# Performance work log

Measured on AMD Instinct MI355X. Metric: run time of the kernel, lower is better.

## Reference

```python
import jax, jax.numpy as jnp
import numpy as np

B, NQ, NK = 8, 1024, 1024
DQ = DK = DV = 512
H = 8
DS = DV // H
EPS = 1e-4
MAX_ITER = 3
SQRT_V = DV ** 0.25  # sqrt(sqrt(dim_V))


def setup_inputs() -> dict:
    key = jax.random.key(0)
    ks = jax.random.split(key, 8)
    s = 0.02
    return {
        "Q": jax.random.normal(ks[0], (B, NQ, DQ), jnp.float32),
        "K": jax.random.normal(ks[1], (B, NK, DK), jnp.float32),
        "Wq": jax.random.normal(ks[2], (DV, DQ), jnp.float32) * s,
        "bq": jnp.zeros((DV,), jnp.float32),
        "Wk": jax.random.normal(ks[3], (DV, DK), jnp.float32) * s,
        "bk": jnp.zeros((DV,), jnp.float32),
        "Wv": jax.random.normal(ks[4], (DV, DK), jnp.float32) * s,
        "bv": jnp.zeros((DV,), jnp.float32),
        "Wo": jax.random.normal(ks[5], (DV, DV), jnp.float32) * s,
        "bo": jnp.zeros((DV,), jnp.float32),
    }


def _split_heads(x):
    # torch.cat(x.split(ds, 2), 0): head-major stacking along batch
    b, n, _ = x.shape
    return x.reshape(b, n, H, DS).transpose(2, 0, 1, 3).reshape(H * b, n, DS)


def _merge_heads(x, b):
    # torch.cat(x.split(b, 0), 2): inverse of _split_heads
    _, n, ds = x.shape
    return x.reshape(H, b, n, ds).transpose(1, 2, 0, 3).reshape(b, n, H * ds)


def _sinkhorn_plan(x, y):
    # x: [M, P1, d], y: [M, P2, d]; cost = pairwise Euclidean (p=2) distance.
    x2 = jnp.sum(x * x, axis=-1)[:, :, None]
    y2 = jnp.sum(y * y, axis=-1)[:, None, :]
    C = jnp.sqrt(jnp.maximum(x2 + y2 - 2.0 * jnp.einsum("mid,mjd->mij", x, y), 0.0))
    m, p1, p2 = C.shape
    log_a = -jnp.log(jnp.float32(p1))  # uniform marginals
    log_b = -jnp.log(jnp.float32(p2))
    u = jnp.zeros((m, p1), C.dtype)
    v = jnp.zeros((m, p2), C.dtype)
    for _ in range(MAX_ITER):  # fixed small iteration count (max_iter=3)
        u = EPS * (log_a - jax.scipy.special.logsumexp((v[:, None, :] - C) / EPS, axis=2))
        v = EPS * (log_b - jax.scipy.special.logsumexp((u[:, :, None] - C) / EPS, axis=1))
    # transport plan P: [M, P1, P2]
    return jnp.exp((u[:, :, None] + v[:, None, :] - C) / EPS)


def reference(Q, K, Wq, bq, Wk, bk, Wv, bv, Wo, bo):
    q = Q @ Wq.T + bq            # [B, NQ, DV]
    k = K @ Wk.T + bk            # [B, NK, DV]
    v = K @ Wv.T + bv            # [B, NK, DV]
    b = Q.shape[0]
    q_, k_, v_ = _split_heads(q), _split_heads(k), _split_heads(v)  # [H*B, N, DS]
    A = _sinkhorn_plan(q_ / SQRT_V, k_ / SQRT_V)                    # [H*B, NQ, NK]
    O = _merge_heads(q_ + jnp.einsum("mij,mjd->mid", A, v_), b)     # [B, NQ, DV]
    return O + jax.nn.relu(O @ Wo.T + bo)
```

## Files before the change

kernel.cpp:

```cpp
#include <hip/hip_runtime.h>
#include <hip/hip_bf16.h>
#include <math.h>

#define NB 8
#define NN 1024
#define ND 512
#define NH 8
#define NDS 64
#define NM 64
#define LOG_A (-6.93147180559945f)
#define SQRT_V 4.75682846001088f
#define INV_SQRT_V 0.210224103813429f
#define INV_EPS 10000.0f
#define L2E  1.44269504088896f
#define LN2F 0.693147180559945f
#define IEL2 14426.9504088896f

#define SPLIT_ELEMS ((size_t)NM * NN * NDS)
#define W_ELEMS     ((size_t)ND * ND)
#define UV_FLOATS   ((size_t)NM * NN)

typedef unsigned short u16;
typedef unsigned int   u32;
typedef __attribute__((ext_vector_type(8))) short bf16x8;
typedef __attribute__((ext_vector_type(4))) float f32x4;

#define MFMA16(a,b,c) __builtin_amdgcn_mfma_f32_16x16x32_bf16(a,b,c,0,0,0)

__device__ __forceinline__ u16 f2bf_t(float x) {
  return (u16)(__float_as_uint(x) >> 16);
}
__device__ __forceinline__ float bf2f(u16 h) {
  return __uint_as_float(((u32)h) << 16);
}
__device__ __forceinline__ float fast_sqrt(float x) {
  float r;
  asm("v_sqrt_f32 %0, %1" : "=v"(r) : "v"(x));
  return r;
}
__device__ __forceinline__ float fast_exp2(float x) {
  float r;
  asm("v_exp_f32 %0, %1" : "=v"(r) : "v"(x));
  return r;
}
__device__ __forceinline__ float max3f(float a, float b, float c) {
  float r;
  asm("v_max3_f32 %0, %1, %2, %3" : "=v"(r) : "v"(a), "v"(b), "v"(c));
  return r;
}
__device__ __forceinline__ void soft_barrier() {
  asm volatile("s_waitcnt lgkmcnt(0)" ::: "memory");
  __builtin_amdgcn_sched_barrier(0);
  __builtin_amdgcn_s_barrier();
  __builtin_amdgcn_sched_barrier(0);
  asm volatile("" ::: "memory");
}

__global__ __launch_bounds__(256) void k_split(
    const float* __restrict__ X, u16* __restrict__ hi, u16* __restrict__ lo)
{
  const size_t i = ((size_t)blockIdx.x * 256 + threadIdx.x) * 4;
  float4 v = *(const float4*)&X[i];
  const float* vp = (const float*)&v;
  u16 h[4], l[4];
#pragma unroll
  for (int j = 0; j < 4; ++j) {
    h[j] = f2bf_t(vp[j]);
    l[j] = f2bf_t(vp[j] - bf2f(h[j]));
  }
  uint2 ph, pl;
  ph.x = (u32)h[0] | ((u32)h[1] << 16);
  ph.y = (u32)h[2] | ((u32)h[3] << 16);
  pl.x = (u32)l[0] | ((u32)l[1] << 16);
  pl.y = (u32)l[2] | ((u32)l[3] << 16);
  *(uint2*)&hi[i] = ph;
  *(uint2*)&lo[i] = pl;
}

__global__ __launch_bounds__(256, 2) void k_proj_mfma(
    const u16* __restrict__ Xh, const u16* __restrict__ Xl,
    const u16* __restrict__ Wh, const u16* __restrict__ Wl,
    const float* __restrict__ bias, u16* __restrict__ oh,
    u16* __restrict__ ol, u16* __restrict__ oT,
    float* __restrict__ nrm, float scale, int mode)
{
  __shared__ __align__(16) u16 Xhs[2][64][72];
  __shared__ __align__(16) u16 Xls[2][64][72];
  __shared__ __align__(16) u16 Whs[2][64][72];
  __shared__ __align__(16) u16 Wls[2][64][72];
  const int t = threadIdx.x;
  const int r0 = blockIdx.x * 64;
  const int h  = blockIdx.y;
  const int c0 = h * 64;
  const int w = t >> 6, l = t & 63;
  const int c = l & 15, kg = l >> 4;
  const int srow = t >> 2;
  const int skoff = (t & 3) * 16;

  const u16* gxh = &Xh[(size_t)(r0 + srow) * ND + skoff];
  const u16* gxl = &Xl[(size_t)(r0 + srow) * ND + skoff];
  const u16* gwh = &Wh[(size_t)(c0 + srow) * ND + skoff];
  const u16* gwl = &Wl[(size_t)(c0 + srow) * ND + skoff];

  bf16x8 rxh0 = *(const bf16x8*)gxh, rxh1 = *(const bf16x8*)(gxh + 8);
  bf16x8 rxl0 = *(const bf16x8*)gxl, rxl1 = *(const bf16x8*)(gxl + 8);
  bf16x8 rwh0 = *(const bf16x8*)gwh, rwh1 = *(const bf16x8*)(gwh + 8);
  bf16x8 rwl0 = *(const bf16x8*)gwl, rwl1 = *(const bf16x8*)(gwl + 8);

  f32x4 acc[4];
#pragma unroll
  for (int cf = 0; cf < 4; ++cf) acc[cf] = (f32x4){0.f, 0.f, 0.f, 0.f};

  for (int kt = 0; kt < 8; ++kt) {
    const int buf = kt & 1;
    *(bf16x8*)&Xhs[buf][srow][skoff]     = rxh0;
    *(bf16x8*)&Xhs[buf][srow][skoff + 8] = rxh1;
    *(bf16x8*)&Xls[buf][srow][skoff]     = rxl0;
    *(bf16x8*)&Xls[buf][srow][skoff + 8] = rxl1;
    *(bf16x8*)&Whs[buf][srow][skoff]     = rwh0;
    *(bf16x8*)&Whs[buf][srow][skoff + 8] = rwh1;
    *(bf16x8*)&Wls[buf][srow][skoff]     = rwl0;
    *(bf16x8*)&Wls[buf][srow][skoff + 8] = rwl1;
    {
      const int nk = ((kt + 1) & 7) * 64;
      rxh0 = *(const bf16x8*)(gxh + nk); rxh1 = *(const bf16x8*)(gxh + nk + 8);
      rxl0 = *(const bf16x8*)(gxl + nk); rxl1 = *(const bf16x8*)(gxl + nk + 8);
      rwh0 = *(const bf16x8*)(gwh + nk); rwh1 = *(const bf16x8*)(gwh + nk + 8);
      rwl0 = *(const bf16x8*)(gwl + nk); rwl1 = *(const bf16x8*)(gwl + nk + 8);
    }
    soft_barrier();
#pragma unroll
    for (int ks = 0; ks < 2; ++ks) {
      bf16x8 Ah = *(const bf16x8*)&Xhs[buf][w * 16 + c][ks * 32 + kg * 8];
      bf16x8 Al = *(const bf16x8*)&Xls[buf][w * 16 + c][ks * 32 + kg * 8];
#pragma unroll
      for (int cf = 0; cf < 4; ++cf) {
        bf16x8 Bh = *(const bf16x8*)&Whs[buf][cf * 16 + c][ks * 32 + kg * 8];
        bf16x8 Bl = *(const bf16x8*)&Wls[buf][cf * 16 + c][ks * 32 + kg * 8];
        acc[cf] = MFMA16(Ah, Bh, acc[cf]);
        acc[cf] = MFMA16(Ah, Bl, acc[cf]);
        acc[cf] = MFMA16(Al, Bh, acc[cf]);
      }
    }
  }

  const int bb = r0 >> 10;
  const int n0 = r0 & 1023;
  const size_t mrow = (size_t)(h * NB + bb) * NN;
  if (mode != 1) {
    float ns[4] = {0.f, 0.f, 0.f, 0.f};
#pragma unroll
    for (int cf = 0; cf < 4; ++cf) {
      const int col = c0 + cf * 16 + c;
      const float bv = bias[col];
#pragma unroll
      for (int r = 0; r < 4; ++r) {
        float v = (acc[cf][r] + bv) * scale;
        u16 hv = f2bf_t(v);
        ns[r] = fmaf(v, v, ns[r]);
        int n = n0 + w * 16 + kg * 4 + r;
        size_t idx = (mrow + n) * NDS + cf * 16 + c;
        oh[idx] = hv;
        if (mode == 0) ol[idx] = f2bf_t(v - bf2f(hv));
      }
    }
#pragma unroll
    for (int off = 1; off <= 8; off <<= 1)
#pragma unroll
      for (int r = 0; r < 4; ++r) ns[r] += __shfl_xor(ns[r], off);
    if (c == 0) {
#pragma unroll
      for (int r = 0; r < 4; ++r)
        nrm[mrow + n0 + w * 16 + kg * 4 + r] = ns[r];
    }
  } else {
#pragma unroll
    for (int cf = 0; cf < 4; ++cf) {
      const int d = cf * 16 + c;
      const float bv = bias[c0 + d];
      u16 p0 = f2bf_t((acc[cf][0] + bv) * scale);
      u16 p1 = f2bf_t((acc[cf][1] + bv) * scale);
      u16 p2 = f2bf_t((acc[cf][2] + bv) * scale);
      u16 p3 = f2bf_t((acc[cf][3] + bv) * scale);
      uint2 p;
      p.x = (u32)p0 | ((u32)p1 << 16);
      p.y = (u32)p2 | ((u32)p3 << 16);
      *(uint2*)&oT[((size_t)(h * NB + bb) * NDS + d) * NN + n0 + w * 16 + kg * 4] = p;
    }
  }
}

__global__ __launch_bounds__(512, 4) void k_lse_mfma(
    const u16* __restrict__ Ah_, const u16* __restrict__ Bh_,
    const float* __restrict__ Anrm, const float* __restrict__ Bnrm,
    const float* __restrict__ din, float* __restrict__ dout, int first)
{
  __shared__ __align__(16) float din_s[NN];
  __shared__ __align__(16) float y2_s[NN];
  __shared__ __align__(16) u16 Bhs[4][64][72];
  const int t = threadIdx.x;
  const int Lb = blockIdx.x;
  const int xcd = Lb & 7, slot = Lb >> 3;
  const int m = xcd + 8 * (slot >> 3);
  const int a0 = (slot & 7) * 128;

  if (first) {
    *(float2*)&din_s[t * 2] = make_float2(0.f, 0.f);
  } else {
    float2 dv = *(const float2*)&din[(size_t)m * NN + t * 2];
    dv.x *= L2E; dv.y *= L2E;
    *(float2*)&din_s[t * 2] = dv;
  }
  *(float2*)&y2_s[t * 2] = *(const float2*)&Bnrm[(size_t)m * NN + t * 2];

  const int w = t >> 6, l = t & 63;
  const int c = l & 15, kg = l >> 4;
  const int arow = a0 + w * 16;
  const size_t mbase = (size_t)m * NN * NDS;

  const u16* pah = &Ah_[mbase + (size_t)(arow + c) * NDS + kg * 8];
  bf16x8 A0h = *(const bf16x8*)pah;
  bf16x8 A1h = *(const bf16x8*)(pah + 32);

  float x2r[4];
#pragma unroll
  for (int r = 0; r < 4; ++r) x2r[r] = Anrm[(size_t)m * NN + arow + kg * 4 + r];
  float M[4], S[4];
#pragma unroll
  for (int r = 0; r < 4; ++r) { M[r] = -3.0e38f; S[r] = 0.f; }

  const int srow = t >> 3;
  const int skoff = (t & 7) * 8;
  const u16* gh = &Bh_[mbase + (size_t)srow * NDS + skoff];
  bf16x8 r0 = *(const bf16x8*)gh;
  bf16x8 r1 = *(const bf16x8*)(gh + 4096);
  __syncthreads();

  for (int bt = 0; bt < 16; bt += 2) {
    const int p2 = (bt >> 1) & 1;
    *(bf16x8*)&Bhs[p2 * 2 + 0][srow][skoff] = r0;
    *(bf16x8*)&Bhs[p2 * 2 + 1][srow][skoff] = r1;
    {
      r0 = *(const bf16x8*)(gh + (size_t)((bt + 2) & 15) * 4096);
      r1 = *(const bf16x8*)(gh + (size_t)((bt + 3) & 15) * 4096);
    }
    soft_barrier();
#pragma unroll
    for (int sub = 0; sub < 2; ++sub) {
      const int b0 = (bt + sub) * 64;
      const int pl = p2 * 2 + sub;
      f32x4 acc[4];
#pragma unroll
      for (int cf = 0; cf < 4; ++cf) {
        const int bl = cf * 16 + c;
        bf16x8 B0h = *(const bf16x8*)&Bhs[pl][bl][kg * 8];
        bf16x8 B1h = *(const bf16x8*)&Bhs[pl][bl][kg * 8 + 32];
        f32x4 a = {0.f, 0.f, 0.f, 0.f};
        a = MFMA16(A0h, B0h, a);
        a = MFMA16(A1h, B1h, a);
        acc[cf] = a;
      }
      float X[4][4];
#pragma unroll
      for (int cf = 0; cf < 4; ++cf) {
        const int col = b0 + cf * 16 + c;
        const float vb2 = din_s[col];
        const float y2  = y2_s[col];
#pragma unroll
        for (int r = 0; r < 4; ++r) {
          float d2 = fmaf(-2.f, acc[cf][r], x2r[r] + y2);
          float sq = fast_sqrt(fmaxf(d2, 0.f));
          X[cf][r] = fmaf(-IEL2, sq, vb2);
        }
      }
#pragma unroll
      for (int r = 0; r < 4; ++r) {
        float m1 = max3f(X[0][r], X[1][r], X[2][r]);
        float nm = max3f(m1, X[3][r], M[r]);
        float s4 = fast_exp2(X[0][r] - nm) + fast_exp2(X[1][r] - nm)
                 + fast_exp2(X[2][r] - nm) + fast_exp2(X[3][r] - nm);
        S[r] = fmaf(S[r], fast_exp2(M[r] - nm), s4);
        M[r] = nm;
      }
    }
  }
#pragma unroll
  for (int off = 1; off <= 8; off <<= 1) {
#pragma unroll
    for (int r = 0; r < 4; ++r) {
      float Mo = __shfl_xor(M[r], off);
      float So = __shfl_xor(S[r], off);
      float nm = fmaxf(M[r], Mo);
      S[r] = S[r] * fast_exp2(M[r] - nm) + So * fast_exp2(Mo - nm);
      M[r] = nm;
    }
  }
  if (c == 0) {
#pragma unroll
    for (int r = 0; r < 4; ++r)
      dout[(size_t)m * NN + arow + kg * 4 + r] =
          LOG_A - M[r] * LN2F - __logf(S[r]);
  }
}

__global__ __launch_bounds__(512, 4) void k_pv_mfma(
    const u16* __restrict__ qh, const u16* __restrict__ ql,
    const u16* __restrict__ kh, const u16* __restrict__ vT,
    const float* __restrict__ qn, const float* __restrict__ kn,
    const float* __restrict__ ue, const float* __restrict__ ve,
    u16* __restrict__ Oh_, u16* __restrict__ Ol_)
{
  __shared__ __align__(16) float ve_s[NN];
  __shared__ __align__(16) float y2_s[NN];
  __shared__ __align__(16) u16 Bhs[2][64][72];
  __shared__ __align__(16) u16 Vs[2][64][72];
  __shared__ __align__(16) u16 pT[8][16][40];
  const int t = threadIdx.x;
  const int Lb = blockIdx.x;
  const int xcd = Lb & 7, slot = Lb >> 3;
  const int m = xcd + 8 * (slot >> 3);
  const int a0 = (slot & 7) * 128;
  {
    float2 vv = *(const float2*)&ve[(size_t)m * NN + t * 2];
    vv.x *= L2E; vv.y *= L2E;
    *(float2*)&ve_s[t * 2] = vv;
  }
  *(float2*)&y2_s[t * 2] = *(const float2*)&kn[(size_t)m * NN + t * 2];

  const int w = t >> 6, l = t & 63;
  const int c = l & 15, kg = l >> 4;
  const int arow = a0 + w * 16;
  const size_t mbase = (size_t)m * NN * NDS;

  const u16* pah = &qh[mbase + (size_t)(arow + c) * NDS + kg * 8];
  bf16x8 A0h = *(const bf16x8*)pah;
  bf16x8 A1h = *(const bf16x8*)(pah + 32);

  float x2r[4], uer2[4];
#pragma unroll
  for (int r = 0; r < 4; ++r) {
    x2r[r]  = qn[(size_t)m * NN + arow + kg * 4 + r];
    uer2[r] = ue[(size_t)m * NN + arow + kg * 4 + r] * L2E;
  }
  f32x4 pacc[4];
#pragma unroll
  for (int df = 0; df < 4; ++df) pacc[df] = (f32x4){0.f, 0.f, 0.f, 0.f};

  const int srow = t >> 3;
  const int skoff = (t & 7) * 8;
  const u16* gh = &kh[mbase + (size_t)srow * NDS + skoff];
  const u16* gv = &vT[((size_t)m * NDS + srow) * NN + skoff];
  bf16x8 rh = *(const bf16x8*)gh;
  bf16x8 rv = *(const bf16x8*)gv;
  __syncthreads();

  for (int bt = 0; bt < 16; ++bt) {
    const int b0 = bt * 64;
    const int buf = bt & 1;
    *(bf16x8*)&Bhs[buf][srow][skoff] = rh;
    *(bf16x8*)&Vs[buf][srow][skoff]  = rv;
    {
      const int nbt = (bt + 1) & 15;
      rh = *(const bf16x8*)(gh + (size_t)nbt * 4096);
      rv = *(const bf16x8*)(gv + (size_t)nbt * 64);
    }
    soft_barrier();
#pragma unroll
    for (int ph = 0; ph < 2; ++ph) {
      f32x4 acc[2];
#pragma unroll
      for (int q = 0; q < 2; ++q) {
        const int cf = ph * 2 + q;
        const int bl = cf * 16 + c;
        bf16x8 B0h = *(const bf16x8*)&Bhs[buf][bl][kg * 8];
        bf16x8 B1h = *(const bf16x8*)&Bhs[buf][bl][kg * 8 + 32];
        f32x4 a = {0.f, 0.f, 0.f, 0.f};
        a = MFMA16(A0h, B0h, a);
        a = MFMA16(A1h, B1h, a);
        acc[q] = a;
      }
#pragma unroll
      for (int q = 0; q < 2; ++q) {
        const int cf = ph * 2 + q;
        const int col = b0 + cf * 16 + c;
        const float ve2 = ve_s[col];
        const float y2  = y2_s[col];
#pragma unroll
        for (int r = 0; r < 4; ++r) {
          float d2 = fmaf(-2.f, acc[q][r], x2r[r] + y2);
          float sq = fast_sqrt(fmaxf(d2, 0.f));
          float p  = fast_exp2(fmaf(-IEL2, sq, uer2[r] + ve2));
          pT[w][kg * 4 + r][q * 16 + c] = f2bf_t(p);
        }
      }
      bf16x8 Pa = *(const bf16x8*)&pT[w][c][kg * 8];
#pragma unroll
      for (int df = 0; df < 4; ++df) {
        bf16x8 Vb = *(const bf16x8*)&Vs[buf][df * 16 + c][ph * 32 + kg * 8];
        pacc[df] = MFMA16(Pa, Vb, pacc[df]);
      }
    }
  }
#pragma unroll
  for (int df = 0; df < 4; ++df) {
#pragma unroll
    for (int r = 0; r < 4; ++r) {
      int row = arow + kg * 4 + r;
      int d = df * 16 + c;
      size_t qi = mbase + (size_t)row * NDS + d;
      float qv = bf2f(qh[qi]) + bf2f(ql[qi]);
      float o  = fmaf(SQRT_V, qv, pacc[df][r]);
      u16 hv = f2bf_t(o);
      Oh_[qi] = hv;
      Ol_[qi] = f2bf_t(o - bf2f(hv));
    }
  }
}

__global__ __launch_bounds__(256, 2) void k_out_mfma(
    const u16* __restrict__ Oh_, const u16* __restrict__ Ol_,
    const u16* __restrict__ Wh, const u16* __restrict__ Wl,
    const float* __restrict__ bo, float* __restrict__ out)
{
  __shared__ __align__(16) u16 Ahs[2][64][72];
  __shared__ __align__(16) u16 Als[2][64][72];
  __shared__ __align__(16) u16 Whs[2][64][72];
  __shared__ __align__(16) u16 Wls[2][64][72];
  const int t = threadIdx.x;
  const int r0 = blockIdx.x * 64;
  const int c0 = blockIdx.y * 64;
  const int bb = r0 >> 10;
  const int n0 = r0 & 1023;
  const int w = t >> 6, l = t & 63;
  const int c = l & 15, kg = l >> 4;
  const int srow = t >> 2;
  const int skoff = (t & 3) * 16;

  f32x4 acc[4];
#pragma unroll
  for (int cf = 0; cf < 4; ++cf) acc[cf] = (f32x4){0.f, 0.f, 0.f, 0.f};

  bf16x8 rah0, rah1, ral0, ral1, rwh0, rwh1, rwl0, rwl1;
  {
    const size_t ob = ((size_t)(0 * NB + bb) * NN + n0 + srow) * NDS;
    const u16* gah = &Oh_[ob + skoff];
    const u16* gal = &Ol_[ob + skoff];
    const u16* gwh = &Wh[(size_t)(c0 + srow) * ND + skoff];
    const u16* gwl = &Wl[(size_t)(c0 + srow) * ND + skoff];
    rah0 = *(const bf16x8*)gah; rah1 = *(const bf16x8*)(gah + 8);
    ral0 = *(const bf16x8*)gal; ral1 = *(const bf16x8*)(gal + 8);
    rwh0 = *(const bf16x8*)gwh; rwh1 = *(const bf16x8*)(gwh + 8);
    rwl0 = *(const bf16x8*)gwl; rwl1 = *(const bf16x8*)(gwl + 8);
  }

  for (int kt = 0; kt < 8; ++kt) {
    const int buf = kt & 1;
    *(bf16x8*)&Ahs[buf][srow][skoff]     = rah0;
    *(bf16x8*)&Ahs[buf][srow][skoff + 8] = rah1;
    *(bf16x8*)&Als[buf][srow][skoff]     = ral0;
    *(bf16x8*)&Als[buf][srow][skoff + 8] = ral1;
    *(bf16x8*)&Whs[buf][srow][skoff]     = rwh0;
    *(bf16x8*)&Whs[buf][srow][skoff + 8] = rwh1;
    *(bf16x8*)&Wls[buf][srow][skoff]     = rwl0;
    *(bf16x8*)&Wls[buf][srow][skoff + 8] = rwl1;
    {
      const int nkt = (kt + 1) & 7;
      const size_t ob = ((size_t)(nkt * NB + bb) * NN + n0 + srow) * NDS;
      const u16* gah = &Oh_[ob + skoff];
      const u16* gal = &Ol_[ob + skoff];
      const u16* gwh = &Wh[(size_t)(c0 + srow) * ND + nkt * 64 + skoff];
      const u16* gwl = &Wl[(size_t)(c0 + srow) * ND + nkt * 64 + skoff];
      rah0 = *(const bf16x8*)gah; rah1 = *(const bf16x8*)(gah + 8);
      ral0 = *(const bf16x8*)gal; ral1 = *(const bf16x8*)(gal + 8);
      rwh0 = *(const bf16x8*)gwh; rwh1 = *(const bf16x8*)(gwh + 8);
      rwl0 = *(const bf16x8*)gwl; rwl1 = *(const bf16x8*)(gwl + 8);
    }
    soft_barrier();
#pragma unroll
    for (int ks = 0; ks < 2; ++ks) {
      bf16x8 Ah = *(const bf16x8*)&Ahs[buf][w * 16 + c][ks * 32 + kg * 8];
      bf16x8 Al = *(const bf16x8*)&Als[buf][w * 16 + c][ks * 32 + kg * 8];
#pragma unroll
      for (int cf = 0; cf < 4; ++cf) {
        bf16x8 Bh = *(const bf16x8*)&Whs[buf][cf * 16 + c][ks * 32 + kg * 8];
        bf16x8 Bl = *(const bf16x8*)&Wls[buf][cf * 16 + c][ks * 32 + kg * 8];
        acc[cf] = MFMA16(Ah, Bh, acc[cf]);
        acc[cf] = MFMA16(Ah, Bl, acc[cf]);
        acc[cf] = MFMA16(Al, Bh, acc[cf]);
      }
    }
  }
#pragma unroll
  for (int cf = 0; cf < 4; ++cf) {
    const int col = c0 + cf * 16 + c;
    const int d = cf * 16 + c;
    const float bv = bo[col];
#pragma unroll
    for (int r = 0; r < 4; ++r) {
      const int n = n0 + w * 16 + kg * 4 + r;
      const size_t oi = ((size_t)(blockIdx.y * NB + bb) * NN + n) * NDS + d;
      float om = bf2f(Oh_[oi]) + bf2f(Ol_[oi]);
      out[(size_t)(r0 + w * 16 + kg * 4 + r) * ND + col] =
          om + fmaxf(acc[cf][r] + bv, 0.f);
    }
  }
}

extern "C" void kernel_launch(void* const* d_in, const int* in_sizes, int n_in,
                              void* d_out, int out_size, void* d_ws, size_t ws_size,
                              hipStream_t stream) {
  const float* Q  = (const float*)d_in[0];
  const float* K  = (const float*)d_in[1];
  const float* Wq = (const float*)d_in[2];
  const float* bq = (const float*)d_in[3];
  const float* Wk = (const float*)d_in[4];
  const float* bk = (const float*)d_in[5];
  const float* Wv = (const float*)d_in[6];
  const float* bv = (const float*)d_in[7];
  const float* Wo = (const float*)d_in[8];
  const float* bo = (const float*)d_in[9];
  float* out = (float*)d_out;

  const size_t need_bytes =
      7 * SPLIT_ELEMS * sizeof(u16) + 8 * W_ELEMS * sizeof(u16) +
      4 * UV_FLOATS * sizeof(float);
  if (ws_size < need_bytes) return;

  u16* qh = (u16*)d_ws;
  u16* ql = qh + SPLIT_ELEMS;
  u16* kh = ql + SPLIT_ELEMS;
  u16* kl = kh + SPLIT_ELEMS;
  u16* vT = kl + SPLIT_ELEMS;
  u16* Oh = vT + SPLIT_ELEMS;
  u16* Ol = Oh + SPLIT_ELEMS;
  u16* wqh = Ol + SPLIT_ELEMS;
  u16* wql = wqh + W_ELEMS;
  u16* wkh = wql + W_ELEMS;
  u16* wkl = wkh + W_ELEMS;
  u16* wvh = wkl + W_ELEMS;
  u16* wvl = wvh + W_ELEMS;
  u16* woh = wvl + W_ELEMS;
  u16* wol = woh + W_ELEMS;
  float* ue = (float*)(wol + W_ELEMS);
  float* ve = ue + UV_FLOATS;
  float* qn = ve + UV_FLOATS;
  float* kn = qn + UV_FLOATS;

  u16* Qrh = Oh;
  u16* Qrl = Ol;
  u16* Krh = (u16*)d_out;
  u16* Krl = Krh + SPLIT_ELEMS;

  dim3 blk(256);
  k_split<<<dim3(4096), blk, 0, stream>>>(Q, Qrh, Qrl);
  k_split<<<dim3(4096), blk, 0, stream>>>(K, Krh, Krl);
  k_split<<<dim3(256), blk, 0, stream>>>(Wq, wqh, wql);
  k_split<<<dim3(256), blk, 0, stream>>>(Wk, wkh, wkl);
  k_split<<<dim3(256), blk, 0, stream>>>(Wv, wvh, wvl);
  k_split<<<dim3(256), blk, 0, stream>>>(Wo, woh, wol);
  k_proj_mfma<<<dim3(128, 8), blk, 0, stream>>>(Qrh, Qrl, wqh, wql, bq, qh, ql, nullptr, qn, INV_SQRT_V, 0);
  k_proj_mfma<<<dim3(128, 8), blk, 0, stream>>>(Krh, Krl, wkh, wkl, bk, kh, nullptr, nullptr, kn, INV_SQRT_V, 2);
  k_proj_mfma<<<dim3(128, 8), blk, 0, stream>>>(Krh, Krl, wvh, wvl, bv, nullptr, nullptr, vT, nullptr, 1.0f, 1);
  for (int it = 0; it < 3; ++it) {
    k_lse_mfma<<<dim3(512), dim3(512), 0, stream>>>(qh, kh, qn, kn, ve, ue, it == 0 ? 1 : 0);
    k_lse_mfma<<<dim3(512), dim3(512), 0, stream>>>(kh, qh, kn, qn, ue, ve, 0);
  }
  k_pv_mfma<<<dim3(512), dim3(512), 0, stream>>>(qh, ql, kh, vT, qn, kn, ue, ve, Oh, Ol);
  k_out_mfma<<<dim3(128, 8), blk, 0, stream>>>(Oh, Ol, woh, wol, bo, out);
}
```

Baseline: 309.8 us.

## Software-pipeline LSE kernel so MFMA of next tile pair overlaps epilogue

Restructures the Sinkhorn logsumexp kernel's main loop into a software pipeline with two accumulator sets. MFMAs for the next pair of 64-column tiles are issued before the sqrt/exp2 epilogue of the previous pair. This lets matrix-core work overlap the transcendental-heavy VALU epilogue instead of running them back to back. In exchange it doubles the live accumulator registers (16 f32x4), which under launch_bounds(512,4) may cause spills or pressure.

```diff
diff --git a/kernel.cpp b/kernel.cpp
--- a/kernel.cpp
+++ b/kernel.cpp
@@ -190,6 +190,59 @@
   }
 }
 
+
+#define LSE_STAGE(PL0, PL1, NP)                                          \
+  *(bf16x8*)&Bhs[PL0][srow][skoff] = r0;                                 \
+  *(bf16x8*)&Bhs[PL1][srow][skoff] = r1;                                 \
+  r0 = *(const bf16x8*)(gh + (size_t)(((NP)*2) & 15) * 4096);            \
+  r1 = *(const bf16x8*)(gh + (size_t)(((NP)*2 + 1) & 15) * 4096);
+
+#define LSE_MFMA_PAIR(ACC, PL0, PL1)                                     \
+  _Pragma("unroll")                                                      \
+  for (int cf = 0; cf < 4; ++cf) {                                       \
+    const int bl = cf * 16 + c;                                          \
+    bf16x8 B0h = *(const bf16x8*)&Bhs[PL0][bl][kg * 8];                  \
+    bf16x8 B1h = *(const bf16x8*)&Bhs[PL0][bl][kg * 8 + 32];             \
+    f32x4 a = {0.f, 0.f, 0.f, 0.f};                                      \
+    a = MFMA16(A0h, B0h, a);                                             \
+    a = MFMA16(A1h, B1h, a);                                             \
+    ACC[cf] = a;                                                         \
+    bf16x8 C0h = *(const bf16x8*)&Bhs[PL1][bl][kg * 8];                  \
+    bf16x8 C1h = *(const bf16x8*)&Bhs[PL1][bl][kg * 8 + 32];             \
+    f32x4 b = {0.f, 0.f, 0.f, 0.f};                                      \
+    b = MFMA16(A0h, C0h, b);                                             \
+    b = MFMA16(A1h, C1h, b);                                             \
+    ACC[4 + cf] = b;                                                     \
+  }
+
+#define LSE_EPI(ACC, PAIR)                                               \
+  _Pragma("unroll")                                                      \
+  for (int sub = 0; sub < 2; ++sub) {                                    \
+    const int b0e = ((PAIR) * 2 + sub) * 64;                             \
+    float X[4][4];                                                       \
+    _Pragma("unroll")                                                    \
+    for (int cf = 0; cf < 4; ++cf) {                                     \
+      const int col = b0e + cf * 16 + c;                                 \
+      const float vb2 = din_s[col];                                      \
+      const float y2e = y2_s[col];                                       \
+      _Pragma("unroll")                                                  \
+      for (int r = 0; r < 4; ++r) {                                      \
+        float d2 = fmaf(-2.f, ACC[sub * 4 + cf][r], x2r[r] + y2e);       \
+        float sq = fast_sqrt(fmaxf(d2, 0.f));                            \
+        X[cf][r] = fmaf(-IEL2, sq, vb2);                                 \
+      }                                                                  \
+    }                                                                    \
+    _Pragma("unroll")                                                    \
+    for (int r = 0; r < 4; ++r) {                                        \
+      float m1 = max3f(X[0][r], X[1][r], X[2][r]);                       \
+      float nm = max3f(m1, X[3][r], M[r]);                               \
+      float s4 = fast_exp2(X[0][r] - nm) + fast_exp2(X[1][r] - nm)       \
+               + fast_exp2(X[2][r] - nm) + fast_exp2(X[3][r] - nm);      \
+      S[r] = fmaf(S[r], fast_exp2(M[r] - nm), s4);                       \
+      M[r] = nm;                                                         \
+    }                                                                    \
+  }
+
 __global__ __launch_bounds__(512, 4) void k_lse_mfma(
     const u16* __restrict__ Ah_, const u16* __restrict__ Bh_,
     const float* __restrict__ Anrm, const float* __restrict__ Bnrm,
@@ -236,54 +289,30 @@
   bf16x8 r1 = *(const bf16x8*)(gh + 4096);
   __syncthreads();
 
-  for (int bt = 0; bt < 16; bt += 2) {
-    const int p2 = (bt >> 1) & 1;
-    *(bf16x8*)&Bhs[p2 * 2 + 0][srow][skoff] = r0;
-    *(bf16x8*)&Bhs[p2 * 2 + 1][srow][skoff] = r1;
-    {
-      r0 = *(const bf16x8*)(gh + (size_t)((bt + 2) & 15) * 4096);
-      r1 = *(const bf16x8*)(gh + (size_t)((bt + 3) & 15) * 4096);
-    }
+  f32x4 accA[8], accB[8];
+
+  LSE_STAGE(0, 1, 1);
+  soft_barrier();
+  LSE_MFMA_PAIR(accA, 0, 1);
+
+#pragma unroll
+  for (int i = 0; i < 3; ++i) {
+    const int bp = 1 + 2 * i;
+    LSE_STAGE(2, 3, bp + 1);
     soft_barrier();
-#pragma unroll
-    for (int sub = 0; sub < 2; ++sub) {
-      const int b0 = (bt + sub) * 64;
-      const int pl = p2 * 2 + sub;
-      f32x4 acc[4];
-#pragma unroll
-      for (int cf = 0; cf < 4; ++cf) {
-        const int bl = cf * 16 + c;
-        bf16x8 B0h = *(const bf16x8*)&Bhs[pl][bl][kg * 8];
-        bf16x8 B1h = *(const bf16x8*)&Bhs[pl][bl][kg * 8 + 32];
-        f32x4 a = {0.f, 0.f, 0.f, 0.f};
-        a = MFMA16(A0h, B0h, a);
-        a = MFMA16(A1h, B1h, a);
-        acc[cf] = a;
-      }
-      float X[4][4];
-#pragma unroll
-      for (int cf = 0; cf < 4; ++cf) {
-        const int col = b0 + cf * 16 + c;
-        const float vb2 = din_s[col];
-        const float y2  = y2_s[col];
-#pragma unroll
-        for (int r = 0; r < 4; ++r) {
-          float d2 = fmaf(-2.f, acc[cf][r], x2r[r] + y2);
-          float sq = fast_sqrt(fmaxf(d2, 0.f));
-          X[cf][r] = fmaf(-IEL2, sq, vb2);
-        }
-      }
-#pragma unroll
-      for (int r = 0; r < 4; ++r) {
-        float m1 = max3f(X[0][r], X[1][r], X[2][r]);
-        float nm = max3f(m1, X[3][r], M[r]);
-        float s4 = fast_exp2(X[0][r] - nm) + fast_exp2(X[1][r] - nm)
-                 + fast_exp2(X[2][r] - nm) + fast_exp2(X[3][r] - nm);
-        S[r] = fmaf(S[r], fast_exp2(M[r] - nm), s4);
-        M[r] = nm;
-      }
-    }
-  }
+    LSE_MFMA_PAIR(accB, 2, 3);
+    LSE_EPI(accA, bp - 1);
+    LSE_STAGE(0, 1, bp + 2);
+    soft_barrier();
+    LSE_MFMA_PAIR(accA, 0, 1);
+    LSE_EPI(accB, bp);
+  }
+  LSE_STAGE(2, 3, 0);
+  soft_barrier();
+  LSE_MFMA_PAIR(accB, 2, 3);
+  LSE_EPI(accA, 6);
+  LSE_EPI(accB, 7);
+
 #pragma unroll
   for (int off = 1; off <= 8; off <<= 1) {
 #pragma unroll
```

New measurement: 317.6 us. +2.5%, slower.
